# Performance work log

Measured on AMD Instinct MI355X. Metric: run time of the kernel, lower is better.

Reference implementation:

```python
import jax, jax.numpy as jnp
import numpy as np
import math

D = 1024
H = 16
NEG = -10000.0


def _layernorm(x, g, b, eps=1e-6):
    mu = x.mean(-1, keepdims=True)
    var = ((x - mu) ** 2).mean(-1, keepdims=True)
    return (x - mu) / jnp.sqrt(var + eps) * g + b


def _gelu(x):
    return x * 0.5 * (1.0 + jax.lax.erf(x / math.sqrt(2.0)))


def _split_heads(x):
    N, L, _ = x.shape
    return x.reshape(N, L, H, D // H).transpose(0, 2, 1, 3)  # (N,H,L,d)


def _attention(q, k, v, mask):
    # q,k,v: (N,Lq/Lk,D); mask: (N,1,Lq,Lk) of 0/1 or None
    d = D // H
    qh, kh, vh = _split_heads(q), _split_heads(k), _split_heads(v)
    scores = jnp.einsum('bhqd,bhkd->bhqk', qh, kh) / math.sqrt(d)
    if mask is not None:
        scores = scores + (1.0 - mask) * NEG
    probs = jax.nn.softmax(scores, axis=-1)
    ctx = jnp.einsum('bhqk,bhkd->bhqd', probs, vh)
    N, _, Lq, _ = ctx.shape
    ctx = ctx.transpose(0, 2, 1, 3).reshape(N, Lq, D)
    return ctx, scores.mean(1)  # attention_vis = masked scaled scores averaged over heads


def setup_inputs() -> dict:
    key = jax.random.key(0)
    ks = jax.random.split(key, 16)
    N, Lt, Lv = 16, 512, 512
    w = lambda k: (jax.random.normal(k, (D, D), jnp.float32) * 0.02)
    inp = {
        'dec_hidden_states': jax.random.normal(ks[0], (N, Lt, D), jnp.float32),
        'dec_mask': jnp.ones((N, Lt), jnp.float32),
        'enc_outputs': jax.random.normal(ks[1], (N, Lv, D), jnp.float32),
        'sa_wq': w(ks[2]), 'sa_bq': jnp.zeros((D,), jnp.float32),
        'sa_wk': w(ks[3]), 'sa_bk': jnp.zeros((D,), jnp.float32),
        'sa_wv': w(ks[4]), 'sa_bv': jnp.zeros((D,), jnp.float32),
        'n1_g': jnp.ones((D,), jnp.float32), 'n1_b': jnp.zeros((D,), jnp.float32),
        'ca_wq': w(ks[5]), 'ca_bq': jnp.zeros((D,), jnp.float32),
        'ca_wk': w(ks[6]), 'ca_bk': jnp.zeros((D,), jnp.float32),
        'ca_wv': w(ks[7]), 'ca_bv': jnp.zeros((D,), jnp.float32),
        'n2_g': jnp.ones((D,), jnp.float32), 'n2_b': jnp.zeros((D,), jnp.float32),
        'int_w': w(ks[8]), 'int_b': jnp.zeros((D,), jnp.float32),
        'out_w': w(ks[9]), 'out_b': jnp.zeros((D,), jnp.float32),
        'out_g': jnp.ones((D,), jnp.float32), 'out_beta': jnp.zeros((D,), jnp.float32),
    }
    return inp


def reference(dec_hidden_states, dec_mask, enc_outputs,
              sa_wq, sa_bq, sa_wk, sa_bk, sa_wv, sa_bv, n1_g, n1_b,
              ca_wq, ca_bq, ca_wk, ca_bk, ca_wv, ca_bv, n2_g, n2_b,
              int_w, int_b, out_w, out_b, out_g, out_beta):
    x = dec_hidden_states
    N, Lt, _ = x.shape
    # causal + padding mask: (N,1,Lt) * tril(Lt,Lt) -> (N,Lt,Lt) -> (N,1,Lt,Lt)
    causal = jnp.tril(jnp.ones((Lt, Lt), x.dtype))
    self_mask = (dec_mask[:, None, :] * causal)[:, None, :, :]
    # self attention
    q = x @ sa_wq + sa_bq
    k = x @ sa_wk + sa_bk
    v = x @ sa_wv + sa_bv
    sa_ctx, _ = _attention(q, k, v, self_mask)
    h = _layernorm(sa_ctx + x, n1_g, n1_b)
    # cross attention (no mask)
    cq = h @ ca_wq + ca_bq
    ck = enc_outputs @ ca_wk + ca_bk
    cv = enc_outputs @ ca_wv + ca_bv
    ca_ctx, attention_vis = _attention(cq, ck, cv, None)
    h2 = _layernorm(h + ca_ctx, n2_g, n2_b)
    # intermediate (gelu FFN)
    inter = _gelu(h2 @ int_w + int_b)
    # Output: dense + residual(intermediate itself, as in original) + LayerNorm
    out = _layernorm(inter @ out_w + out_b + inter, out_g, out_beta)
    return out, attention_vis
```

## Files before the change

### kernel.cpp

```cpp
#include <hip/hip_runtime.h>
#include <hip/hip_bf16.h>
#include <math.h>

#define DDIM 1024
#define NH   16
#define LTOK 512
#define NBATCH 16

typedef unsigned short u16;
typedef unsigned short u16x8 __attribute__((ext_vector_type(8)));
typedef unsigned short u16x4 __attribute__((ext_vector_type(4)));
typedef __bf16 bf16x8 __attribute__((ext_vector_type(8)));
typedef float f32x4 __attribute__((ext_vector_type(4)));

typedef __attribute__((address_space(1))) void as1_void;
typedef __attribute__((address_space(3))) void as3_void;

__device__ __forceinline__ void llds16(const u16* g, u16* l) {
    __builtin_amdgcn_global_load_lds((as1_void*)g, (as3_void*)l, 16, 0, 0);
}

__device__ __forceinline__ float bf2f(u16 u) {
    unsigned v = ((unsigned)u) << 16;
    float f; __builtin_memcpy(&f, &v, 4); return f;
}
__device__ __forceinline__ u16 f2bf(float f) {
    unsigned u; __builtin_memcpy(&u, &f, 4);
    u += 0x7fffu + ((u >> 16) & 1u);
    return (u16)(u >> 16);
}

__global__ __launch_bounds__(256) void gemm_bt_kernel(
    const u16* __restrict__ A, int lda, long sA1, long sA2,
    const u16* __restrict__ B, int ldb, long sB1, long sB2,
    u16* __restrict__ C, float* __restrict__ Cf, int ldc, long sC1, long sC2,
    int M, int N, int K, int zdiv,
    const float* __restrict__ bias, float scale, int flags)
{
    __shared__ __align__(16) u16 As[128 * 32];
    __shared__ __align__(16) u16 Bs[128 * 32];

    const int z  = blockIdx.y;
    const int zb = z / zdiv, zh = z - zb * zdiv;
    const u16* Ab = A + (long)zb * sA1 + (long)zh * sA2;
    const u16* Bb = B + (long)zb * sB1 + (long)zh * sB2;
    u16*   Cb  = C  ? C  + (long)zb * sC1 + (long)zh * sC2 : nullptr;
    float* Cfb = Cf ? Cf + (long)zb * sC1 + (long)zh * sC2 : nullptr;

    const int tilesN = (N + 127) >> 7;
    const int tm = blockIdx.x / tilesN, tn = blockIdx.x - tm * tilesN;
    const int m0 = tm << 7, n0 = tn << 7;

    const int tid  = threadIdx.x;
    const int lane = tid & 63;
    const int wave = tid >> 6;
    const int wm = (wave & 1) << 6, wn = (wave >> 1) << 6;
    const int quad = lane >> 4, l16 = lane & 15;

    f32x4 acc[4][4];
#pragma unroll
    for (int i = 0; i < 4; i++)
#pragma unroll
        for (int j = 0; j < 4; j++) acc[i][j] = (f32x4){0.f, 0.f, 0.f, 0.f};

    const int lrA = (wave << 5) + (lane >> 2);
    const int lc  = (lane & 3) << 3;
    int ra0 = m0 + lrA;      if (ra0 > M - 1) ra0 = M - 1;
    int ra1 = m0 + lrA + 16; if (ra1 > M - 1) ra1 = M - 1;
    int rb0 = n0 + lrA;      if (rb0 > N - 1) rb0 = N - 1;
    int rb1 = n0 + lrA + 16; if (rb1 > N - 1) rb1 = N - 1;
    const u16* gA0 = Ab + (long)ra0 * lda + lc;
    const u16* gA1 = Ab + (long)ra1 * lda + lc;
    const u16* gB0 = Bb + (long)rb0 * ldb + lc;
    const u16* gB1 = Bb + (long)rb1 * ldb + lc;
    u16* lA0 = As + ((wave << 5) +  0) * 32;
    u16* lA1 = As + ((wave << 5) + 16) * 32;
    u16* lB0 = Bs + ((wave << 5) +  0) * 32;
    u16* lB1 = Bs + ((wave << 5) + 16) * 32;

    for (int k0 = 0; k0 < K; k0 += 32) {
        __syncthreads();
        llds16(gA0 + k0, lA0);
        llds16(gA1 + k0, lA1);
        llds16(gB0 + k0, lB0);
        llds16(gB1 + k0, lB1);
        __syncthreads();

        bf16x8 af[4], bfr[4];
#pragma unroll
        for (int t = 0; t < 4; t++)
            af[t] = *(const bf16x8*)(As + (wm + t * 16 + l16) * 32 + quad * 8);
#pragma unroll
        for (int t = 0; t < 4; t++)
            bfr[t] = *(const bf16x8*)(Bs + (wn + t * 16 + l16) * 32 + quad * 8);
#pragma unroll
        for (int i = 0; i < 4; i++)
#pragma unroll
            for (int j = 0; j < 4; j++)
                acc[i][j] = __builtin_amdgcn_mfma_f32_16x16x32_bf16(
                    af[i], bfr[j], acc[i][j], 0, 0, 0);
    }

#pragma unroll
    for (int j = 0; j < 4; j++) {
        int col  = n0 + wn + j * 16 + l16;
        int colc = col < N ? col : N - 1;
        float bv = bias ? bias[colc] : 0.f;
#pragma unroll
        for (int i = 0; i < 4; i++) {
#pragma unroll
            for (int r = 0; r < 4; r++) {
                int row = m0 + wm + i * 16 + quad * 4 + r;
                float v = acc[i][j][r] * scale + bv;
                if (flags & 1)
                    v = 0.5f * v * (1.f + erff(v * 0.70710678118654752f));
                if (row < M && col < N) {
                    if (Cfb) Cfb[(long)row * ldc + col] = v;
                    else     Cb [(long)row * ldc + col] = f2bf(v);
                }
            }
        }
    }
}

__global__ __launch_bounds__(256, 4) void flash_kernel(
    const u16* __restrict__ Q, const u16* __restrict__ K,
    const u16* __restrict__ VT, u16* __restrict__ O,
    const float* __restrict__ mask, int causal)
{
    __shared__ __align__(16) u16 Ks[128 * 72];
    __shared__ __align__(16) u16 Vs[64 * 136];
    const int tid  = threadIdx.x;
    const int wave = tid >> 6, lane = tid & 63;
    const int quad = lane >> 4, l16 = lane & 15;
    const int bh = blockIdx.x, qt = blockIdx.y, b = bh >> 4, h = bh & 15;
    const int qbase = qt * 64 + wave * 16;
    const int qrow  = qbase + l16;

    const u16* qp = Q + ((long)b * LTOK + qrow) * DDIM + h * 64 + quad * 8;
    bf16x8 aq0 = *(const bf16x8*)(qp);
    bf16x8 aq1 = *(const bf16x8*)(qp + 32);

    f32x4 oacc[4];
#pragma unroll
    for (int jd = 0; jd < 4; jd++) oacc[jd] = (f32x4){0.f, 0.f, 0.f, 0.f};
    float m_st = -3.0e38f;
    float l_st = 0.f;

    const int krow = tid >> 3,       kcol = (tid & 7) << 3;
    const int vrow = tid >> 2,       vcol = (tid & 3) << 3;
    const u16* gK = K + ((long)b * LTOK + krow) * DDIM + h * 64 + kcol;
    const u16* gV = VT + ((long)bh * 64 + vrow) * LTOK + vcol;

    const float C1    = 0.125f * 1.44269504088896340736f;
    const float NEGL2 = -10000.0f * 1.44269504088896340736f;

    const int jp    = quad >> 1;
    const int laneA = ((quad & 1) << 5) | l16;

    const int nkt = causal ? ((qt * 64 + 63) >> 7) + 1 : (LTOK >> 7);
    for (int kt = 0; kt < nkt; kt++) {
        const int k0 = kt << 7;

        __syncthreads();
#pragma unroll
        for (int i = 0; i < 4; i++)
            *(u16x8*)(Ks + (i * 32 + krow) * 72 + kcol) =
                *(const u16x8*)(gK + (long)(k0 + i * 32) * DDIM);
#pragma unroll
        for (int i = 0; i < 4; i++)
            *(u16x8*)(Vs + vrow * 136 + i * 32 + vcol) =
                *(const u16x8*)(gV + k0 + i * 32);
        __syncthreads();

        f32x4 s[8];
#pragma unroll
        for (int j = 0; j < 8; j++) {
            bf16x8 bk0 = *(const bf16x8*)(Ks + (j * 16 + l16) * 72 + quad * 8);
            bf16x8 bk1 = *(const bf16x8*)(Ks + (j * 16 + l16) * 72 + 32 + quad * 8);
            f32x4 z = (f32x4){0.f, 0.f, 0.f, 0.f};
            z = __builtin_amdgcn_mfma_f32_16x16x32_bf16(bk0, aq0, z, 0, 0, 0);
            s[j] = __builtin_amdgcn_mfma_f32_16x16x32_bf16(bk1, aq1, z, 0, 0, 0);
        }

        float tm0 = -3.0e38f, tm1 = -3.0e38f, tm2 = -3.0e38f, tm3 = -3.0e38f;
#pragma unroll
        for (int j = 0; j < 8; j++) {
            if (causal) {
                f32x4 m4 = *(const f32x4*)(mask + (long)b * LTOK + k0 + j * 16 + quad * 4);
#pragma unroll
                for (int r = 0; r < 4; r++) {
                    int key = k0 + j * 16 + quad * 4 + r;
                    float ad = (key <= qrow) ? fmaf(m4[r], -NEGL2, NEGL2) : NEGL2;
                    s[j][r] = fmaf(s[j][r], C1, ad);
                }
            } else {
#pragma unroll
                for (int r = 0; r < 4; r++) s[j][r] *= C1;
            }
            tm0 = fmaxf(tm0, s[j][0]); tm1 = fmaxf(tm1, s[j][1]);
            tm2 = fmaxf(tm2, s[j][2]); tm3 = fmaxf(tm3, s[j][3]);
        }
        float tmax = fmaxf(fmaxf(tm0, tm1), fmaxf(tm2, tm3));
        tmax = fmaxf(tmax, __shfl_xor(tmax, 16));
        tmax = fmaxf(tmax, __shfl_xor(tmax, 32));

        float mnew  = fmaxf(m_st, tmax);
        float alpha = __builtin_amdgcn_exp2f(m_st - mnew);
        m_st = mnew;

        float rs0 = 0.f, rs1 = 0.f, rs2 = 0.f, rs3 = 0.f;
        unsigned pk[8][2];
#pragma unroll
        for (int j = 0; j < 8; j++) {
            float p0 = __builtin_amdgcn_exp2f(s[j][0] - mnew);
            float p1 = __builtin_amdgcn_exp2f(s[j][1] - mnew);
            float p2 = __builtin_amdgcn_exp2f(s[j][2] - mnew);
            float p3 = __builtin_amdgcn_exp2f(s[j][3] - mnew);
            rs0 += p0; rs1 += p1; rs2 += p2; rs3 += p3;
            asm("v_cvt_pk_bf16_f32 %0, %1, %2" : "=v"(pk[j][0]) : "v"(p0), "v"(p1));
            asm("v_cvt_pk_bf16_f32 %0, %1, %2" : "=v"(pk[j][1]) : "v"(p2), "v"(p3));
        }
        float rsum = (rs0 + rs1) + (rs2 + rs3);
        rsum += __shfl_xor(rsum, 16);
        rsum += __shfl_xor(rsum, 32);
        l_st = l_st * alpha + rsum;

#pragma unroll
        for (int jd = 0; jd < 4; jd++) oacc[jd] *= alpha;

#pragma unroll
        for (int kk = 0; kk < 4; kk++) {
            unsigned e0 = __shfl(pk[2 * kk][0],     laneA);
            unsigned e1 = __shfl(pk[2 * kk][1],     laneA);
            unsigned o0 = __shfl(pk[2 * kk + 1][0], laneA);
            unsigned o1 = __shfl(pk[2 * kk + 1][1], laneA);
            unsigned w0 = jp ? o0 : e0;
            unsigned w1 = jp ? o1 : e1;
            e0 = __shfl(pk[2 * kk][0],     laneA + 16);
            e1 = __shfl(pk[2 * kk][1],     laneA + 16);
            o0 = __shfl(pk[2 * kk + 1][0], laneA + 16);
            o1 = __shfl(pk[2 * kk + 1][1], laneA + 16);
            unsigned w2 = jp ? o0 : e0;
            unsigned w3 = jp ? o1 : e1;
            unsigned wv[4] = {w0, w1, w2, w3};
            bf16x8 bp; __builtin_memcpy(&bp, wv, 16);
#pragma unroll
            for (int jd = 0; jd < 4; jd++) {
                bf16x8 av = *(const bf16x8*)(Vs + (jd * 16 + l16) * 136
                                                + kk * 32 + quad * 8);
                oacc[jd] = __builtin_amdgcn_mfma_f32_16x16x32_bf16(av, bp, oacc[jd], 0, 0, 0);
            }
        }
    }

    float linv = 1.f / l_st;
    long obase = ((long)b * LTOK + qrow) * DDIM + h * 64;
#pragma unroll
    for (int jd = 0; jd < 4; jd++) {
        u16x4 ov;
#pragma unroll
        for (int r = 0; r < 4; r++) ov[r] = f2bf(oacc[jd][r] * linv);
        *(u16x4*)(O + obase + jd * 16 + quad * 4) = ov;
    }
}

__global__ __launch_bounds__(256) void add_ln_kernel(
    const u16* __restrict__ a, const u16* __restrict__ b,
    const float* __restrict__ b32,
    const float* __restrict__ g, const float* __restrict__ bt,
    u16* __restrict__ o, float* __restrict__ of)
{
    long row = blockIdx.x;
    int tid = threadIdx.x;
    __shared__ float red[4];
    const u16* ar = a + row * DDIM;
    float xv[4]; float s = 0.f;
#pragma unroll
    for (int i = 0; i < 4; i++) {
        int c = tid + 256 * i;
        float sum = bf2f(ar[c]) + (b32 ? b32[row * DDIM + c] : bf2f(b[row * DDIM + c]));
        xv[i] = fminf(fmaxf(sum, -1.0e18f), 1.0e18f);
        s += xv[i];
    }
#pragma unroll
    for (int ofs = 32; ofs >= 1; ofs >>= 1) s += __shfl_xor(s, ofs);
    int wave = tid >> 6, lane = tid & 63;
    if (lane == 0) red[wave] = s;
    __syncthreads();
    float mu = (red[0] + red[1] + red[2] + red[3]) * (1.f / 1024.f);
    __syncthreads();
    float v = 0.f;
#pragma unroll
    for (int i = 0; i < 4; i++) { float d = xv[i] - mu; v += d * d; }
#pragma unroll
    for (int ofs = 32; ofs >= 1; ofs >>= 1) v += __shfl_xor(v, ofs);
    if (lane == 0) red[wave] = v;
    __syncthreads();
    float var = (red[0] + red[1] + red[2] + red[3]) * (1.f / 1024.f);
    float inv = rsqrtf(var + 1e-6f);
#pragma unroll
    for (int i = 0; i < 4; i++) {
        int c = tid + 256 * i;
        float r = (xv[i] - mu) * inv * g[c] + bt[c];
        if (of) of[row * DDIM + c] = r;
        else    o [row * DDIM + c] = f2bf(r);
    }
}

__global__ __launch_bounds__(256) void cvt_kernel(
    const float* __restrict__ src, u16* __restrict__ dst)
{
    long i = ((long)blockIdx.x * 256 + threadIdx.x) * 8;
    u16x8 o;
#pragma unroll
    for (int j = 0; j < 8; j++) o[j] = f2bf(src[i + j]);
    *(u16x8*)(dst + i) = o;
}

__global__ __launch_bounds__(256) void wt_kernel(
    const float* w0, const float* w1, const float* w2, const float* w3,
    const float* w4, const float* w5, const float* w6, const float* w7,
    u16* __restrict__ wt)
{
    const float* srcs[8] = {w0, w1, w2, w3, w4, w5, w6, w7};
    const float* w = srcs[blockIdx.z];
    u16* o = wt + (long)blockIdx.z * DDIM * DDIM;
    __shared__ u16 t[32][33];
    int tx = threadIdx.x & 31, ty = threadIdx.x >> 5;
    int c0 = blockIdx.x << 5, r0 = blockIdx.y << 5;
#pragma unroll
    for (int i = 0; i < 4; i++)
        t[ty + 8 * i][tx] = f2bf(w[(long)(r0 + ty + 8 * i) * DDIM + c0 + tx]);
    __syncthreads();
#pragma unroll
    for (int i = 0; i < 4; i++)
        o[(long)(c0 + ty + 8 * i) * DDIM + r0 + tx] = t[tx][ty + 8 * i];
}

__global__ __launch_bounds__(256) void vtrans_kernel(
    const u16* __restrict__ v, u16* __restrict__ vt)
{
    int bh = blockIdx.y; int b = bh >> 4, h = bh & 15;
    int k0 = blockIdx.x << 5;
    __shared__ __align__(16) u16 t[32 * 72];
    int kk = threadIdx.x >> 3, c = (threadIdx.x & 7) << 3;
    u16x8 val = *(const u16x8*)(v + ((long)b * LTOK + k0 + kk) * DDIM + h * 64 + c);
    *(u16x8*)(t + kk * 72 + c) = val;
    __syncthreads();
    int dd = threadIdx.x >> 2, k2 = (threadIdx.x & 3) << 3;
    u16x8 o;
#pragma unroll
    for (int j = 0; j < 8; j++) o[j] = t[(k2 + j) * 72 + dd];
    *(u16x8*)(vt + ((long)bh * 64 + dd) * LTOK + k0 + k2) = o;
}

extern "C" void kernel_launch(void* const* d_in, const int* in_sizes, int n_in,
                              void* d_out, int out_size, void* d_ws, size_t ws_size,
                              hipStream_t stream)
{
    const float* x     = (const float*)d_in[0];
    const float* dmsk  = (const float*)d_in[1];
    const float* enc   = (const float*)d_in[2];
    const float* sa_wq = (const float*)d_in[3];  const float* sa_bq = (const float*)d_in[4];
    const float* sa_wk = (const float*)d_in[5];  const float* sa_bk = (const float*)d_in[6];
    const float* sa_wv = (const float*)d_in[7];  const float* sa_bv = (const float*)d_in[8];
    const float* n1_g  = (const float*)d_in[9];  const float* n1_b  = (const float*)d_in[10];
    const float* ca_wq = (const float*)d_in[11]; const float* ca_bq = (const float*)d_in[12];
    const float* ca_wk = (const float*)d_in[13]; const float* ca_bk = (const float*)d_in[14];
    const float* ca_wv = (const float*)d_in[15]; const float* ca_bv = (const float*)d_in[16];
    const float* n2_g  = (const float*)d_in[17]; const float* n2_b  = (const float*)d_in[18];
    const float* int_w = (const float*)d_in[19]; const float* int_b = (const float*)d_in[20];
    const float* out_w = (const float*)d_in[21]; const float* out_b = (const float*)d_in[22];
    const float* out_g = (const float*)d_in[23]; const float* out_bt= (const float*)d_in[24];

    float* outp = (float*)d_out;
    float* visp = outp + (long)NBATCH * LTOK * DDIM;

    const size_t WTB  = (size_t)8 * DDIM * DDIM * 2;
    const size_t BUF1 = (size_t)LTOK * DDIM * 2;
    int cb = 16;
    while (cb > 1 && WTB + (size_t)cb * 7 * BUF1 + 8192 > ws_size)
        cb >>= 1;

    char* ws = (char*)d_ws;
    size_t off = 0;
    auto alloc = [&](size_t bytes) -> u16* {
        u16* p = (u16*)(ws + off);
        off += (bytes + 255) & ~(size_t)255;
        return p;
    };
    u16* Bq  = alloc((size_t)cb * BUF1);
    u16* Bk  = alloc((size_t)cb * BUF1);
    u16* Bv  = alloc((size_t)cb * BUF1);
    u16* Bt  = alloc((size_t)cb * BUF1);
    u16* Bt2 = alloc((size_t)cb * BUF1);
    u16* Xb  = alloc((size_t)cb * BUF1);
    u16* Eb  = alloc((size_t)cb * BUF1);
    u16* WT  = alloc(WTB);

    u16* Wsaq = WT + 0L * DDIM * DDIM; u16* Wsak = WT + 1L * DDIM * DDIM;
    u16* Wsav = WT + 2L * DDIM * DDIM; u16* Wcaq = WT + 3L * DDIM * DDIM;
    u16* Wcak = WT + 4L * DDIM * DDIM; u16* Wcav = WT + 5L * DDIM * DDIM;
    u16* Wint = WT + 6L * DDIM * DDIM; u16* Wout = WT + 7L * DDIM * DDIM;

    auto gemm = [&](const u16* A, int lda, long sA1, long sA2,
                    const u16* B, int ldb, long sB1, long sB2,
                    u16* C, float* Cf, int ldc, long sC1, long sC2,
                    int M, int N, int K, int Z, int zdiv,
                    const float* bias, float scale, int flags) {
        int tM = (M + 127) / 128, tN = (N + 127) / 128;
        gemm_bt_kernel<<<dim3(tM * tN, Z), dim3(256), 0, stream>>>(
            A, lda, sA1, sA2, B, ldb, sB1, sB2, C, Cf, ldc, sC1, sC2,
            M, N, K, zdiv, bias, scale, flags);
    };

    const long SLD = (long)LTOK * DDIM;
    const long SSC = (long)LTOK * LTOK;

    wt_kernel<<<dim3(32, 32, 8), dim3(256), 0, stream>>>(
        sa_wq, sa_wk, sa_wv, ca_wq, ca_wk, ca_wv, int_w, out_w, WT);

    for (int b0 = 0; b0 < NBATCH; b0 += cb) {
        const float* xc = x   + (long)b0 * SLD;
        const float* ec = enc + (long)b0 * SLD;
        const int M = cb * LTOK;
        const int Z = cb * NH;
        const int cvtg = (int)(((long)M * DDIM) / (256 * 8));

        cvt_kernel<<<dim3(cvtg), dim3(256), 0, stream>>>(xc, Xb);
        cvt_kernel<<<dim3(cvtg), dim3(256), 0, stream>>>(ec, Eb);

        gemm(Xb, DDIM, 0, 0, Wsaq, DDIM, 0, 0, Bq, nullptr, DDIM, 0, 0, M, DDIM, DDIM, 1, 1, sa_bq, 1.f, 0);
        gemm(Xb, DDIM, 0, 0, Wsak, DDIM, 0, 0, Bk, nullptr, DDIM, 0, 0, M, DDIM, DDIM, 1, 1, sa_bk, 1.f, 0);
        gemm(Xb, DDIM, 0, 0, Wsav, DDIM, 0, 0, Bv, nullptr, DDIM, 0, 0, M, DDIM, DDIM, 1, 1, sa_bv, 1.f, 0);
        vtrans_kernel<<<dim3(16, Z), dim3(256), 0, stream>>>(Bv, Bt);

        flash_kernel<<<dim3(Z, 8), dim3(256), 0, stream>>>(
            Bq, Bk, Bt, Bv, dmsk + (long)b0 * LTOK, 1);

        add_ln_kernel<<<dim3(M), dim3(256), 0, stream>>>(
            Bv, nullptr, xc, n1_g, n1_b, Bq, nullptr);

        gemm(Bq, DDIM, 0, 0, Wcaq, DDIM, 0, 0, Bk, nullptr, DDIM, 0, 0, M, DDIM, DDIM, 1, 1, ca_bq, 1.f, 0);
        gemm(Eb, DDIM, 0, 0, Wcak, DDIM, 0, 0, Bv, nullptr, DDIM, 0, 0, M, DDIM, DDIM, 1, 1, ca_bk, 1.f, 0);
        gemm(Eb, DDIM, 0, 0, Wcav, DDIM, 0, 0, Bt, nullptr, DDIM, 0, 0, M, DDIM, DDIM, 1, 1, ca_bv, 1.f, 0);

        gemm(Bk, DDIM, SLD, 0, Bv, DDIM, SLD, 0,
             nullptr, visp + (long)b0 * SSC, LTOK, SSC, 0,
             LTOK, LTOK, DDIM, cb, 1, nullptr, 1.f / 128.f, 0);

        vtrans_kernel<<<dim3(16, Z), dim3(256), 0, stream>>>(Bt, Bt2);
        flash_kernel<<<dim3(Z, 8), dim3(256), 0, stream>>>(
            Bk, Bv, Bt2, Bt, nullptr, 0);

        add_ln_kernel<<<dim3(M), dim3(256), 0, stream>>>(
            Bq, Bt, nullptr, n2_g, n2_b, Bv, nullptr);

        gemm(Bv, DDIM, 0, 0, Wint, DDIM, 0, 0, Bk, nullptr, DDIM, 0, 0, M, DDIM, DDIM, 1, 1, int_b, 1.f, 1);
        gemm(Bk, DDIM, 0, 0, Wout, DDIM, 0, 0, Bt, nullptr, DDIM, 0, 0, M, DDIM, DDIM, 1, 1, out_b, 1.f, 0);
        add_ln_kernel<<<dim3(M), dim3(256), 0, stream>>>(
            Bt, Bk, nullptr, out_g, out_bt, nullptr, outp + (long)b0 * SLD);
    }
}
```

Before: 650.6 us.

## Prefetch next K/V tile into registers, drop P shuffles, XCD-aware GEMM tile mapping

```diff
diff --git a/kernel.cpp b/kernel.cpp
--- a/kernel.cpp
+++ b/kernel.cpp
@@ -48,7 +48,17 @@
     float* Cfb = Cf ? Cf + (long)zb * sC1 + (long)zh * sC2 : nullptr;
 
     const int tilesN = (N + 127) >> 7;
-    const int tm = blockIdx.x / tilesN, tn = blockIdx.x - tm * tilesN;
+    const int tilesM = (M + 127) >> 7;
+    int tm, tn;
+    if ((tilesM & 7) == 0) {
+        const int xcd = blockIdx.x & 7, idx = blockIdx.x >> 3;
+        const int mg  = tilesM >> 3;
+        tm = ((idx % mg) << 3) | xcd;
+        tn = idx / mg;
+    } else {
+        tm = blockIdx.x / tilesN;
+        tn = blockIdx.x - tm * tilesN;
+    }
     const int m0 = tm << 7, n0 = tn << 7;
 
     const int tid  = threadIdx.x;
@@ -155,23 +165,34 @@
     const float C1    = 0.125f * 1.44269504088896340736f;
     const float NEGL2 = -10000.0f * 1.44269504088896340736f;
 
-    const int jp    = quad >> 1;
-    const int laneA = ((quad & 1) << 5) | l16;
-
     const int nkt = causal ? ((qt * 64 + 63) >> 7) + 1 : (LTOK >> 7);
+
+    u16x8 KR[4], VR[4];
+#pragma unroll
+    for (int i = 0; i < 4; i++) KR[i] = *(const u16x8*)(gK + (long)(i * 32) * DDIM);
+#pragma unroll
+    for (int i = 0; i < 4; i++) VR[i] = *(const u16x8*)(gV + i * 32);
+#pragma unroll
+    for (int i = 0; i < 4; i++)
+        *(u16x8*)(Ks + (i * 32 + krow) * 72 + kcol) = KR[i];
+#pragma unroll
+    for (int i = 0; i < 4; i++)
+        *(u16x8*)(Vs + vrow * 136 + i * 32 + vcol) = VR[i];
+    __syncthreads();
+
     for (int kt = 0; kt < nkt; kt++) {
         const int k0 = kt << 7;
-
-        __syncthreads();
-#pragma unroll
-        for (int i = 0; i < 4; i++)
-            *(u16x8*)(Ks + (i * 32 + krow) * 72 + kcol) =
-                *(const u16x8*)(gK + (long)(k0 + i * 32) * DDIM);
-#pragma unroll
-        for (int i = 0; i < 4; i++)
-            *(u16x8*)(Vs + vrow * 136 + i * 32 + vcol) =
-                *(const u16x8*)(gV + k0 + i * 32);
-        __syncthreads();
+        const bool more = (kt + 1 < nkt);
+
+        if (more) {
+            const int kn = k0 + 128;
+#pragma unroll
+            for (int i = 0; i < 4; i++)
+                KR[i] = *(const u16x8*)(gK + (long)(kn + i * 32) * DDIM);
+#pragma unroll
+            for (int i = 0; i < 4; i++)
+                VR[i] = *(const u16x8*)(gV + kn + i * 32);
+        }
 
         f32x4 s[8];
 #pragma unroll
@@ -231,26 +252,29 @@
 
 #pragma unroll
         for (int kk = 0; kk < 4; kk++) {
-            unsigned e0 = __shfl(pk[2 * kk][0],     laneA);
-            unsigned e1 = __shfl(pk[2 * kk][1],     laneA);
-            unsigned o0 = __shfl(pk[2 * kk + 1][0], laneA);
-            unsigned o1 = __shfl(pk[2 * kk + 1][1], laneA);
-            unsigned w0 = jp ? o0 : e0;
-            unsigned w1 = jp ? o1 : e1;
-            e0 = __shfl(pk[2 * kk][0],     laneA + 16);
-            e1 = __shfl(pk[2 * kk][1],     laneA + 16);
-            o0 = __shfl(pk[2 * kk + 1][0], laneA + 16);
-            o1 = __shfl(pk[2 * kk + 1][1], laneA + 16);
-            unsigned w2 = jp ? o0 : e0;
-            unsigned w3 = jp ? o1 : e1;
-            unsigned wv[4] = {w0, w1, w2, w3};
+            unsigned wv[4] = { pk[2 * kk][0], pk[2 * kk][1],
+                               pk[2 * kk + 1][0], pk[2 * kk + 1][1] };
             bf16x8 bp; __builtin_memcpy(&bp, wv, 16);
 #pragma unroll
             for (int jd = 0; jd < 4; jd++) {
-                bf16x8 av = *(const bf16x8*)(Vs + (jd * 16 + l16) * 136
-                                                + kk * 32 + quad * 8);
+                const u16* vb = Vs + (jd * 16 + l16) * 136 + kk * 32 + quad * 4;
+                u16 va[8];
+                *(u16x4*)(va)     = *(const u16x4*)(vb);
+                *(u16x4*)(va + 4) = *(const u16x4*)(vb + 16);
+                bf16x8 av; __builtin_memcpy(&av, va, 16);
                 oacc[jd] = __builtin_amdgcn_mfma_f32_16x16x32_bf16(av, bp, oacc[jd], 0, 0, 0);
             }
+        }
+
+        if (more) {
+            __syncthreads();
+#pragma unroll
+            for (int i = 0; i < 4; i++)
+                *(u16x8*)(Ks + (i * 32 + krow) * 72 + kcol) = KR[i];
+#pragma unroll
+            for (int i = 0; i < 4; i++)
+                *(u16x8*)(Vs + vrow * 136 + i * 32 + vcol) = VR[i];
+            __syncthreads();
         }
     }
 
```

After: 616.2 us. 5.3% less time.
